# Kernel tuning notes

Measured on AMD Instinct MI355X. Metric: run time of the kernel, lower is better.

The kernel has to match this reference:

```python
import jax, jax.numpy as jnp
import numpy as np

B, C, H, W = 32, 256, 64, 64
MIP, OUP = 8, 256
BN_EPS = 1e-5


def setup_inputs() -> dict:
    key = jax.random.key(0)
    ks = jax.random.split(key, 8)
    x = jax.random.normal(ks[0], (B, C, H, W), dtype=jnp.float32)
    # 1x1 conv weights stored as (out_ch, in_ch); BN in eval mode (running stats)
    w1 = jax.random.normal(ks[1], (MIP, C), dtype=jnp.float32) * 0.05
    bn_gamma = jnp.ones((MIP,), jnp.float32)
    bn_beta = jnp.zeros((MIP,), jnp.float32)
    bn_mean = jax.random.normal(ks[2], (MIP,), dtype=jnp.float32) * 0.1
    bn_var = jax.random.uniform(ks[3], (MIP,), dtype=jnp.float32) + 0.5
    wh = jax.random.normal(ks[4], (OUP, MIP), dtype=jnp.float32) * 0.1
    ww = jax.random.normal(ks[5], (OUP, MIP), dtype=jnp.float32) * 0.1
    return {"x": x, "w1": w1, "bn_gamma": bn_gamma, "bn_beta": bn_beta,
            "bn_mean": bn_mean, "bn_var": bn_var, "wh": wh, "ww": ww}


def _hswish(y):
    return y * jnp.clip(y + 3.0, 0.0, 6.0) / 6.0


def reference(x, w1, bn_gamma, bn_beta, bn_mean, bn_var, wh, ww):
    b, c, h, w = x.shape
    identity = x
    # Shift (mode='max'): pooled softmax profiles, outer product bias map
    bias_h = jax.nn.softmax(jnp.max(x, axis=3, keepdims=True), axis=2)  # (b,c,h,1)
    bias_w = jax.nn.softmax(jnp.max(x, axis=2, keepdims=True), axis=3)  # (b,c,1,w)
    xb = x + bias_h * bias_w  # outer product via broadcast == matmul((h,1),(1,w))
    # avg-pool profiles, concat along spatial axis -> (b,c,h+w,1)
    a_h = jnp.mean(xb, axis=3, keepdims=True)                 # (b,c,h,1)
    a_w = jnp.mean(xb, axis=2, keepdims=True).transpose(0, 1, 3, 2)  # (b,c,w,1)
    y = jnp.concatenate([a_h, a_w], axis=2)                   # (b,c,h+w,1)
    # 1x1 conv -> BN (eval) -> h_swish
    y = jnp.einsum('mc,bcsl->bmsl', w1, y)
    scale = (bn_gamma / jnp.sqrt(bn_var + BN_EPS)).reshape(1, -1, 1, 1)
    shift = (bn_beta - bn_mean * bn_gamma / jnp.sqrt(bn_var + BN_EPS)).reshape(1, -1, 1, 1)
    y = _hswish(y * scale + shift)
    # split, 1x1 convs, sigmoid gates
    y_h, y_w = y[:, :, :h], y[:, :, h:]
    g_h = jax.nn.sigmoid(jnp.einsum('om,bmhl->bohl', wh, y_h))               # (b,oup,h,1)
    g_w = jax.nn.sigmoid(jnp.einsum('om,bmwl->bowl', ww, y_w)).transpose(0, 1, 3, 2)  # (b,oup,1,w)
    return identity * g_w * g_h
```

## Files before the change

### kernel.cpp

```cpp
#include <hip/hip_runtime.h>
#include <math.h>

#define Bn 32
#define Cn 256
#define Hn 64
#define Wn 64
#define MIP 8
#define OUP 256
#define BN_EPS 1e-5f

__global__ __launch_bounds__(256) void stats_kernel(const float* __restrict__ x,
                                                    float* __restrict__ A) {
    const int bc = blockIdx.x;
    const float* xp = x + (size_t)bc * (Hn * Wn);
    __shared__ float tile[Hn * 65];
    const int t = threadIdx.x;

#pragma unroll
    for (int k = 0; k < 4; ++k) {
        int i4  = t + 256 * k;
        int idx = i4 * 4;
        int h = idx >> 6;
        int w = idx & 63;
        float4 v = ((const float4*)xp)[i4];
        float* dst = &tile[h * 65 + w];
        dst[0] = v.x; dst[1] = v.y; dst[2] = v.z; dst[3] = v.w;
    }
    __syncthreads();

    float red_max = -INFINITY, red_sum = 0.f;
    if (t < 64) {
        int h = t;
#pragma unroll 8
        for (int w = 0; w < Wn; ++w) {
            float v = tile[h * 65 + w];
            red_max = fmaxf(red_max, v);
            red_sum += v;
        }
    } else if (t < 128) {
        int w = t - 64;
#pragma unroll 8
        for (int h = 0; h < Hn; ++h) {
            float v = tile[h * 65 + w];
            red_max = fmaxf(red_max, v);
            red_sum += v;
        }
    }

    if (t < 128) {
        float m = red_max;
#pragma unroll
        for (int off = 32; off > 0; off >>= 1) m = fmaxf(m, __shfl_xor(m, off));
        float e = expf(red_max - m);
        float se = e;
#pragma unroll
        for (int off = 32; off > 0; off >>= 1) se += __shfl_xor(se, off);
        float a = (red_sum + e / se) * (1.0f / 64.0f);
        A[(size_t)bc * 128 + t] = a;
    }
}

__global__ __launch_bounds__(256) void ymix_kernel(const float* __restrict__ A,
                                                   const float* __restrict__ w1,
                                                   const float* __restrict__ bn_gamma,
                                                   const float* __restrict__ bn_beta,
                                                   const float* __restrict__ bn_mean,
                                                   const float* __restrict__ bn_var,
                                                   float* __restrict__ yact) {
    const int b = blockIdx.x;
    const int t = threadIdx.x;
    const int s    = t & 127;
    const int half = t >> 7;

    const float* Ab = A + (size_t)b * Cn * 128;

    float acc[MIP];
#pragma unroll
    for (int m = 0; m < MIP; ++m) acc[m] = 0.f;

    const int c0 = half * 128;
    for (int c = c0; c < c0 + 128; ++c) {
        float a = Ab[(size_t)c * 128 + s];
#pragma unroll
        for (int m = 0; m < MIP; ++m)
            acc[m] += w1[m * Cn + c] * a;
    }

    __shared__ float red[MIP][128];
    if (half == 1) {
#pragma unroll
        for (int m = 0; m < MIP; ++m) red[m][s] = acc[m];
    }
    __syncthreads();
    if (half == 0) {
#pragma unroll
        for (int m = 0; m < MIP; ++m) {
            float v = acc[m] + red[m][s];
            float sc = bn_gamma[m] * rsqrtf(bn_var[m] + BN_EPS);
            float sh = bn_beta[m] - bn_mean[m] * sc;
            v = v * sc + sh;
            v = v * fminf(fmaxf(v + 3.0f, 0.0f), 6.0f) * (1.0f / 6.0f);
            yact[(size_t)b * (MIP * 128) + m * 128 + s] = v;
        }
    }
}

__global__ __launch_bounds__(256) void apply_kernel(const float* __restrict__ x,
                                                    const float* __restrict__ yact,
                                                    const float* __restrict__ wh,
                                                    const float* __restrict__ ww,
                                                    float* __restrict__ out) {
    const int bc = blockIdx.x;
    const int b  = bc >> 8;
    const int c  = bc & 255;
    const float* xp = x + (size_t)bc * (Hn * Wn);
    float* op = out + (size_t)bc * (Hn * Wn);

    __shared__ float gs[128];
    const int t = threadIdx.x;
    if (t < 128) {
        const float* w2row = (t < 64) ? (wh + c * MIP) : (ww + c * MIP);
        const float* yb = yact + (size_t)b * (MIP * 128);
        float g = 0.f;
#pragma unroll
        for (int m = 0; m < MIP; ++m)
            g += w2row[m] * yb[m * 128 + t];
        gs[t] = 1.0f / (1.0f + expf(-g));
    }
    __syncthreads();

#pragma unroll
    for (int k = 0; k < 4; ++k) {
        int i4  = t + 256 * k;
        int idx = i4 * 4;
        int h = idx >> 6;
        int w = idx & 63;
        float4 v = ((const float4*)xp)[i4];
        float gh = gs[h];
        v.x *= gh * gs[64 + w + 0];
        v.y *= gh * gs[64 + w + 1];
        v.z *= gh * gs[64 + w + 2];
        v.w *= gh * gs[64 + w + 3];
        ((float4*)op)[i4] = v;
    }
}

extern "C" void kernel_launch(void* const* d_in, const int* in_sizes, int n_in,
                              void* d_out, int out_size, void* d_ws, size_t ws_size,
                              hipStream_t stream) {
    const float* x        = (const float*)d_in[0];
    const float* w1       = (const float*)d_in[1];
    const float* bn_gamma = (const float*)d_in[2];
    const float* bn_beta  = (const float*)d_in[3];
    const float* bn_mean  = (const float*)d_in[4];
    const float* bn_var   = (const float*)d_in[5];
    const float* wh       = (const float*)d_in[6];
    const float* ww       = (const float*)d_in[7];
    float* out = (float*)d_out;

    float* A    = (float*)d_ws;
    float* yact = A + (size_t)Bn * Cn * 128;

    stats_kernel<<<Bn * Cn, 256, 0, stream>>>(x, A);
    ymix_kernel<<<Bn, 256, 0, stream>>>(A, w1, bn_gamma, bn_beta, bn_mean,
                                        bn_var, yact);
    apply_kernel<<<Bn * Cn, 256, 0, stream>>>(x, yact, wh, ww, out);
}
```

Before: 298.4 us.

## Widen ymix reduction to 1024 threads, use fast exp and nontemporal stores

The channel-mix kernel now runs 1024 threads per batch, splitting the 256-channel reduction into eight chunks combined through shared memory instead of two, which shortens its serial loop. The stats and apply kernels switch expf to __expf. The apply kernel writes its output with nontemporal vector stores so the streamed output does not displace cached data. This trades a little exp accuracy and more shared-memory use in the small kernel for lower latency and less cache pollution.

Measured after the change: 268.5 us. 10.0% less time.

```diff
diff --git a/kernel.cpp b/kernel.cpp
--- a/kernel.cpp
+++ b/kernel.cpp
@@ -8,6 +8,8 @@
 #define MIP 8
 #define OUP 256
 #define BN_EPS 1e-5f
+
+typedef float vfloat4 __attribute__((ext_vector_type(4)));
 
 __global__ __launch_bounds__(256) void stats_kernel(const float* __restrict__ x,
                                                     float* __restrict__ A) {
@@ -51,7 +53,7 @@
         float m = red_max;
 #pragma unroll
         for (int off = 32; off > 0; off >>= 1) m = fmaxf(m, __shfl_xor(m, off));
-        float e = expf(red_max - m);
+        float e = __expf(red_max - m);
         float se = e;
 #pragma unroll
         for (int off = 32; off > 0; off >>= 1) se += __shfl_xor(se, off);
@@ -60,17 +62,17 @@
     }
 }
 
-__global__ __launch_bounds__(256) void ymix_kernel(const float* __restrict__ A,
-                                                   const float* __restrict__ w1,
-                                                   const float* __restrict__ bn_gamma,
-                                                   const float* __restrict__ bn_beta,
-                                                   const float* __restrict__ bn_mean,
-                                                   const float* __restrict__ bn_var,
-                                                   float* __restrict__ yact) {
+__global__ __launch_bounds__(1024) void ymix_kernel(const float* __restrict__ A,
+                                                    const float* __restrict__ w1,
+                                                    const float* __restrict__ bn_gamma,
+                                                    const float* __restrict__ bn_beta,
+                                                    const float* __restrict__ bn_mean,
+                                                    const float* __restrict__ bn_var,
+                                                    float* __restrict__ yact) {
     const int b = blockIdx.x;
     const int t = threadIdx.x;
-    const int s    = t & 127;
-    const int half = t >> 7;
+    const int s     = t & 127;
+    const int chunk = t >> 7;
 
     const float* Ab = A + (size_t)b * Cn * 128;
 
@@ -78,24 +80,26 @@
 #pragma unroll
     for (int m = 0; m < MIP; ++m) acc[m] = 0.f;
 
-    const int c0 = half * 128;
-    for (int c = c0; c < c0 + 128; ++c) {
+    const int c0 = chunk * 32;
+    for (int c = c0; c < c0 + 32; ++c) {
         float a = Ab[(size_t)c * 128 + s];
 #pragma unroll
         for (int m = 0; m < MIP; ++m)
             acc[m] += w1[m * Cn + c] * a;
     }
 
-    __shared__ float red[MIP][128];
-    if (half == 1) {
+    __shared__ float red[7][MIP][128];
+    if (chunk > 0) {
 #pragma unroll
-        for (int m = 0; m < MIP; ++m) red[m][s] = acc[m];
+        for (int m = 0; m < MIP; ++m) red[chunk - 1][m][s] = acc[m];
     }
     __syncthreads();
-    if (half == 0) {
+    if (chunk == 0) {
 #pragma unroll
         for (int m = 0; m < MIP; ++m) {
-            float v = acc[m] + red[m][s];
+            float v = acc[m];
+#pragma unroll
+            for (int k = 0; k < 7; ++k) v += red[k][m][s];
             float sc = bn_gamma[m] * rsqrtf(bn_var[m] + BN_EPS);
             float sh = bn_beta[m] - bn_mean[m] * sc;
             v = v * sc + sh;
@@ -125,7 +129,7 @@
 #pragma unroll
         for (int m = 0; m < MIP; ++m)
             g += w2row[m] * yb[m * 128 + t];
-        gs[t] = 1.0f / (1.0f + expf(-g));
+        gs[t] = 1.0f / (1.0f + __expf(-g));
     }
     __syncthreads();
 
@@ -137,11 +141,12 @@
         int w = idx & 63;
         float4 v = ((const float4*)xp)[i4];
         float gh = gs[h];
-        v.x *= gh * gs[64 + w + 0];
-        v.y *= gh * gs[64 + w + 1];
-        v.z *= gh * gs[64 + w + 2];
-        v.w *= gh * gs[64 + w + 3];
-        ((float4*)op)[i4] = v;
+        vfloat4 r;
+        r.x = v.x * gh * gs[64 + w + 0];
+        r.y = v.y * gh * gs[64 + w + 1];
+        r.z = v.z * gh * gs[64 + w + 2];
+        r.w = v.w * gh * gs[64 + w + 3];
+        __builtin_nontemporal_store(r, &((vfloat4*)op)[i4]);
     }
 }
 
@@ -162,7 +167,7 @@
     float* yact = A + (size_t)Bn * Cn * 128;
 
     stats_kernel<<<Bn * Cn, 256, 0, stream>>>(x, A);
-    ymix_kernel<<<Bn, 256, 0, stream>>>(A, w1, bn_gamma, bn_beta, bn_mean,
-                                        bn_var, yact);
+    ymix_kernel<<<Bn, 1024, 0, stream>>>(A, w1, bn_gamma, bn_beta, bn_mean,
+                                         bn_var, yact);
     apply_kernel<<<Bn * Cn, 256, 0, stream>>>(x, yact, wh, ww, out);
 }
```
